# Performance work log

Measured on AMD Instinct MI355X. Metric: run time of the kernel, lower is better.

The kernel has to match this reference:

```python
import jax, jax.numpy as jnp
import numpy as np
import math

B, S, D = 1, 4096, 2048
H, KVH, HD = 16, 4, 128
ROPE_THETA = 10000.0


def _rope_tables(seq_len, head_dim, theta):
    inv_freq = 1.0 / (theta ** (jnp.arange(0, head_dim, 2, dtype=jnp.float32) / head_dim))
    t = jnp.arange(seq_len, dtype=jnp.float32)
    freqs = jnp.outer(t, inv_freq)                      # [S, HD/2]
    emb = jnp.concatenate([freqs, freqs], axis=-1)      # [S, HD]
    return jnp.cos(emb)[None, None], jnp.sin(emb)[None, None]  # [1,1,S,HD]


def setup_inputs() -> dict:
    key = jax.random.key(0)
    ks = jax.random.split(key, 8)
    hidden_states = jax.random.normal(ks[0], (B, S, D), dtype=jnp.float32)
    # additive causal mask [B,1,S,S]
    neg = jnp.finfo(jnp.float32).min
    causal = jnp.where(jnp.tril(jnp.ones((S, S), dtype=bool)), 0.0, neg)
    attention_mask = jnp.broadcast_to(causal[None, None], (B, 1, S, S)).astype(jnp.float32)
    cos, sin = _rope_tables(S, HD, ROPE_THETA)
    gate = jax.random.uniform(ks[1], (B, S), dtype=jnp.float32, minval=0.05, maxval=1.0)
    sc = lambda fan_in: 1.0 / math.sqrt(fan_in)
    Wq = jax.random.normal(ks[2], (D, H * HD), dtype=jnp.float32) * sc(D)
    Wk = jax.random.normal(ks[3], (D, KVH * HD), dtype=jnp.float32) * sc(D)
    Wv = jax.random.normal(ks[4], (D, KVH * HD), dtype=jnp.float32) * sc(D)
    Wo = jax.random.normal(ks[5], (H * HD, D), dtype=jnp.float32) * sc(H * HD)
    return {"hidden_states": hidden_states, "attention_mask": attention_mask,
            "cos": cos, "sin": sin, "gate": gate,
            "Wq": Wq, "Wk": Wk, "Wv": Wv, "Wo": Wo}


def _rotate_half(x):
    h = x.shape[-1] // 2
    return jnp.concatenate([-x[..., h:], x[..., :h]], axis=-1)


def reference(hidden_states, attention_mask, cos, sin, gate, Wq, Wk, Wv, Wo):
    bsz, q_len, _ = hidden_states.shape
    # projections -> [B, heads, S, HD]
    q = (hidden_states @ Wq).reshape(bsz, q_len, H, HD).transpose(0, 2, 1, 3)
    k = (hidden_states @ Wk).reshape(bsz, q_len, KVH, HD).transpose(0, 2, 1, 3)
    v = (hidden_states @ Wv).reshape(bsz, q_len, KVH, HD).transpose(0, 2, 1, 3)
    # inline RoPE
    q = q * cos + _rotate_half(q) * sin
    k = k * cos + _rotate_half(k) * sin
    # GQA: repeat-interleave kv heads to match q heads
    g = H // KVH
    k = jnp.repeat(k, g, axis=1)
    v = jnp.repeat(v, g, axis=1)
    scores = jnp.einsum('bhqd,bhkd->bhqk', q, k) / math.sqrt(HD)
    scores = scores + attention_mask
    scores = scores + jnp.log(gate + 1e-8)[:, None, None, :]  # gate over kv positions
    weights = jax.nn.softmax(scores.astype(jnp.float32), axis=-1).astype(q.dtype)
    out = jnp.einsum('bhqk,bhkd->bhqd', weights, v)
    out = out.transpose(0, 2, 1, 3).reshape(bsz, q_len, H * HD)
    return out @ Wo
```

## Files before the change

### kernel.cpp

```cpp
#include <hip/hip_runtime.h>
#include <math.h>

#define S_LEN 4096
#define DMODEL 2048
#define NH 16
#define NKVH 4
#define HD 128
#define LDQKV 3072

typedef __attribute__((ext_vector_type(4))) float f32x4;
typedef __attribute__((ext_vector_type(8))) short bf16x8;
typedef __attribute__((ext_vector_type(4))) unsigned short us4;

static __device__ __forceinline__ unsigned short f2bf(float f) {
  unsigned int u = __builtin_bit_cast(unsigned int, f);
  u += 0x7fffu + ((u >> 16) & 1u);
  return (unsigned short)(u >> 16);
}
static __device__ __forceinline__ float bf2f(unsigned short h) {
  unsigned int u = ((unsigned int)h) << 16;
  return __builtin_bit_cast(float, u);
}
static __device__ __forceinline__ unsigned int cvt_pk_bf16(float lo, float hi) {
  unsigned int r;
  asm("v_cvt_pk_bf16_f32 %0, %1, %2" : "=v"(r) : "v"(lo), "v"(hi));
  return r;
}

#define GLDS16(g, l) __builtin_amdgcn_global_load_lds( \
    (__attribute__((address_space(1))) void*)(g), \
    (__attribute__((address_space(3))) void*)(l), 16, 0, 0)


__global__ __launch_bounds__(256) void k_cast_bf16(const float* __restrict__ src,
                                                   unsigned short* __restrict__ dst, int n4) {
  int i = blockIdx.x * 256 + threadIdx.x;
  if (i >= n4) return;
  const float4* s = (const float4*)src;
  float4 v = s[i];
  us4 o = { f2bf(v.x), f2bf(v.y), f2bf(v.z), f2bf(v.w) };
  *(us4*)(dst + (size_t)i * 4) = o;
}

__global__ __launch_bounds__(256) void k_transpose_bf16(const float* __restrict__ src,
    unsigned short* __restrict__ dst, int K, int N) {
  __shared__ float tile[64][65];
  int k0 = blockIdx.x * 64, n0 = blockIdx.y * 64;
  int t = threadIdx.x;
#pragma unroll
  for (int i = 0; i < 16; ++i) {
    int idx = t + i * 256;
    int r = idx >> 6, c = idx & 63;
    tile[r][c] = src[(size_t)(k0 + r) * N + n0 + c];
  }
  __syncthreads();
#pragma unroll
  for (int i = 0; i < 16; ++i) {
    int idx = t + i * 256;
    int r = idx >> 6, c = idx & 63;
    dst[(size_t)(n0 + r) * K + k0 + c] = f2bf(tile[c][r]);
  }
}

__global__ __launch_bounds__(256) void k_rope(unsigned short* __restrict__ QKV,
    const float* __restrict__ cp, const float* __restrict__ sp) {
  int gid = blockIdx.x * 256 + threadIdx.x;
  int d = gid & 63;
  int hh = (gid >> 6) % 20;
  int s = gid / 1280;
  int col = hh < NH ? hh * HD : DMODEL + (hh - NH) * HD;
  float qs = hh < NH ? 0.12751589341664477f : 1.0f;
  size_t base = (size_t)s * LDQKV + col;
  float x1 = bf2f(QKV[base + d]);
  float x2 = bf2f(QKV[base + d + 64]);
  float c1 = cp[s * HD + d], s1 = sp[s * HD + d];
  float c2 = cp[s * HD + d + 64], s2 = sp[s * HD + d + 64];
  QKV[base + d]      = f2bf((x1 * c1 - x2 * s1) * qs);
  QKV[base + d + 64] = f2bf((x2 * c2 + x1 * s2) * qs);
}

__global__ __launch_bounds__(256) void k_transpose_v(const unsigned short* __restrict__ QKV,
    unsigned short* __restrict__ Vt) {
  __shared__ unsigned short tile[64][72];
  int s0 = blockIdx.x * 64, c0 = blockIdx.y * 64;
  int t = threadIdx.x;
#pragma unroll
  for (int i = 0; i < 16; ++i) {
    int idx = t + i * 256;
    int r = idx >> 6, c = idx & 63;
    tile[r][c] = QKV[(size_t)(s0 + r) * LDQKV + DMODEL + NKVH * HD + c0 + c];
  }
  __syncthreads();
#pragma unroll
  for (int i = 0; i < 16; ++i) {
    int idx = t + i * 256;
    int r = idx >> 6, c = idx & 63;
    int pc = (c & 3) * 16 + (c >> 2);
    Vt[(size_t)(c0 + r) * S_LEN + s0 + c] = tile[pc][r];
  }
}


template<int OUTF32>
__global__ __launch_bounds__(256) void k_gemm_bt(
    const unsigned short* __restrict__ A, const unsigned short* __restrict__ Bt,
    void* __restrict__ Cp, int M, int N, int K) {
  __shared__ __attribute__((aligned(16))) unsigned short As[128 * 32];
  __shared__ __attribute__((aligned(16))) unsigned short Bs[128 * 32];
  const int t = threadIdx.x;
  const int wave = t >> 6, lane = t & 63;
  const int lr = lane & 15, lg = lane >> 4;
  const int bm = blockIdx.x * 128, bn = blockIdx.y * 128;
  const int wr = (wave >> 1) * 64, wc = (wave & 1) * 64;
  f32x4 acc[4][4];
#pragma unroll
  for (int i = 0; i < 4; ++i)
#pragma unroll
    for (int j = 0; j < 4; ++j) acc[i][j] = (f32x4){0.f, 0.f, 0.f, 0.f};

  for (int k0 = 0; k0 < K; k0 += 32) {
    __syncthreads();
#pragma unroll
    for (int i = 0; i < 2; ++i) {
      const int cb = (wave * 2 + i) * 64;
      const int c = cb + lane;
      const int row = c >> 2, kc = c & 3;
      const int ksw = (kc ^ (row & 3)) * 8;
      GLDS16(A + (size_t)(bm + row) * K + k0 + ksw, (char*)As + cb * 16);
      GLDS16(Bt + (size_t)(bn + row) * K + k0 + ksw, (char*)Bs + cb * 16);
    }
    asm volatile("s_waitcnt vmcnt(0)" ::: "memory");
    __syncthreads();
    bf16x8 af[4], bfr[4];
#pragma unroll
    for (int mi = 0; mi < 4; ++mi) {
      const int row = wr + mi * 16 + lr;
      af[mi] = *(const bf16x8*)(As + row * 32 + ((lg ^ (lr & 3)) * 8));
    }
#pragma unroll
    for (int ni = 0; ni < 4; ++ni) {
      const int row = wc + ni * 16 + lr;
      bfr[ni] = *(const bf16x8*)(Bs + row * 32 + ((lg ^ (lr & 3)) * 8));
    }
#pragma unroll
    for (int mi = 0; mi < 4; ++mi)
#pragma unroll
      for (int ni = 0; ni < 4; ++ni)
        acc[mi][ni] = __builtin_amdgcn_mfma_f32_16x16x32_bf16(af[mi], bfr[ni], acc[mi][ni], 0, 0, 0);
  }
#pragma unroll
  for (int mi = 0; mi < 4; ++mi)
#pragma unroll
    for (int ni = 0; ni < 4; ++ni)
#pragma unroll
      for (int r = 0; r < 4; ++r) {
        const int m = bm + wr + mi * 16 + lg * 4 + r;
        const int n = bn + wc + ni * 16 + lr;
        if (OUTF32) ((float*)Cp)[(size_t)m * N + n] = acc[mi][ni][r];
        else ((unsigned short*)Cp)[(size_t)m * N + n] = f2bf(acc[mi][ni][r]);
      }
}


#define STAGE_KV(kt_, buf_) do { \
  const int kv0_ = (kt_) * 64; \
  _Pragma("unroll") \
  for (int i_ = 0; i_ < 4; ++i_) { \
    const int cb_ = (wave * 4 + i_) * 64; \
    const int c_ = cb_ + lane; \
    { const int row_ = c_ >> 4, kc_ = c_ & 15; \
      GLDS16(Kp + (size_t)(kv0_ + row_) * LDQKV + ((kc_ ^ (row_ & 7)) * 8), \
             (char*)Ks[buf_] + cb_ * 16); } \
    { const int d_ = c_ >> 3, kc_ = c_ & 7; \
      GLDS16(Vp + (size_t)d_ * S_LEN + kv0_ + ((kc_ ^ (d_ & 7)) * 8), \
             (char*)Vs[buf_] + cb_ * 16); } \
  } \
} while (0)

template<bool DIAG>
__device__ __forceinline__ void attn_tile(
    const unsigned short* Kb, const unsigned short* Vb,
    unsigned short (*PsW)[72], const float* __restrict__ gate,
    int kv0, int qbase, const bf16x8* qf,
    f32x4* acc, f32x4& acc_s, float* mrow, int lr, int lg,
    const bf16x8 vb_ones) {
  float g4[4];
#pragma unroll
  for (int cf = 0; cf < 4; ++cf) g4[cf] = gate[kv0 + cf * 16 + lr];

  f32x4 sc[4];
  __builtin_amdgcn_s_setprio(1);
#pragma unroll
  for (int cf = 0; cf < 4; ++cf) {
    sc[cf] = (f32x4){0.f, 0.f, 0.f, 0.f};
    const int row = cf * 16 + lr;
#pragma unroll
    for (int ks = 0; ks < 4; ++ks) {
      bf16x8 kb = *(const bf16x8*)(Kb + row * 128 + (((ks * 4 + lg) ^ (lr & 7)) * 8));
      sc[cf] = __builtin_amdgcn_mfma_f32_16x16x32_bf16(qf[ks], kb, sc[cf], 0, 0, 0);
    }
  }
  __builtin_amdgcn_s_setprio(0);

  if (DIAG) {
#pragma unroll
    for (int cf = 0; cf < 4; ++cf) {
      const int kpos = kv0 + cf * 16 + lr;
#pragma unroll
      for (int r = 0; r < 4; ++r)
        sc[cf][r] = (kpos <= qbase + r) ? sc[cf][r] : -3e38f;
    }
  }
  float lmax[4];
#pragma unroll
  for (int r = 0; r < 4; ++r)
    lmax[r] = fmaxf(fmaxf(sc[0][r], sc[1][r]), fmaxf(sc[2][r], sc[3][r]));

  bool need = (lmax[0] > mrow[0] + 11.5416f) | (lmax[1] > mrow[1] + 11.5416f) |
              (lmax[2] > mrow[2] + 11.5416f) | (lmax[3] > mrow[3] + 11.5416f);
  if (__any(need)) {
    float tm[4] = {lmax[0], lmax[1], lmax[2], lmax[3]};
#pragma unroll
    for (int off = 8; off; off >>= 1)
#pragma unroll
      for (int r = 0; r < 4; ++r) tm[r] = fmaxf(tm[r], __shfl_xor(tm[r], off));
#pragma unroll
    for (int r = 0; r < 4; ++r) {
      const float mn = fmaxf(mrow[r], tm[r]);
      const float alpha = __builtin_amdgcn_exp2f(mrow[r] - mn);
      mrow[r] = mn;
#pragma unroll
      for (int j = 0; j < 8; ++j) acc[j][r] *= alpha;
      acc_s[r] *= alpha;
    }
  }
#pragma unroll
  for (int r = 0; r < 4; ++r) {
    float p0 = __builtin_amdgcn_exp2f(sc[0][r] - mrow[r]) * g4[0];
    float p1 = __builtin_amdgcn_exp2f(sc[1][r] - mrow[r]) * g4[1];
    float p2 = __builtin_amdgcn_exp2f(sc[2][r] - mrow[r]) * g4[2];
    float p3 = __builtin_amdgcn_exp2f(sc[3][r] - mrow[r]) * g4[3];
    uint2 pk = { cvt_pk_bf16(p0, p1), cvt_pk_bf16(p2, p3) };
    *(uint2*)(&PsW[lg * 4 + r][lr * 4]) = pk;
  }
  asm volatile("s_waitcnt lgkmcnt(0)" ::: "memory");
  __builtin_amdgcn_sched_barrier(0);
  __builtin_amdgcn_s_setprio(1);
#pragma unroll
  for (int ks = 0; ks < 2; ++ks) {
    bf16x8 pa = *(const bf16x8*)(&PsW[lr][ks * 32 + lg * 8]);
#pragma unroll
    for (int j = 0; j < 8; ++j) {
      const int d = j * 16 + lr;
      bf16x8 vb = *(const bf16x8*)(Vb + d * 64 + (((ks * 4 + lg) ^ (lr & 7)) * 8));
      acc[j] = __builtin_amdgcn_mfma_f32_16x16x32_bf16(pa, vb, acc[j], 0, 0, 0);
    }
    acc_s = __builtin_amdgcn_mfma_f32_16x16x32_bf16(pa, vb_ones, acc_s, 0, 0, 0);
  }
  __builtin_amdgcn_s_setprio(0);
}

__global__ __launch_bounds__(256) void k_attn(
    const unsigned short* __restrict__ QKV, const unsigned short* __restrict__ Vt,
    const float* __restrict__ gate, unsigned short* __restrict__ Oattn) {
  __shared__ __attribute__((aligned(16))) unsigned short Ks[2][64 * 128];
  __shared__ __attribute__((aligned(16))) unsigned short Vs[2][128 * 64];
  __shared__ __attribute__((aligned(16))) unsigned short Ps[4][16][72];
  const int h = blockIdx.y, kvh = h >> 2;
  const int bx = blockIdx.x;
  const int t = threadIdx.x, wave = t >> 6, lane = t & 63;
  const int lr = lane & 15, lg = lane >> 4;
  const unsigned short* Qp = QKV + h * HD;
  const unsigned short* Kp = QKV + DMODEL + kvh * HD;
  const unsigned short* Vp = Vt + (size_t)kvh * HD * S_LEN;
  unsigned short (*PsW)[72] = Ps[wave];
  bf16x8 vb_ones;
  {
    const short one = (short)0x3F80, z = 0;
    const short e = (lr == 0) ? one : z;
    vb_ones = (bf16x8){e, e, e, e, e, e, e, e};
  }

  for (int half = 0; half < 2; ++half) {
    const int qt = half ? bx : (63 - bx);
    const int q0 = qt * 64;
    const int nt = qt + 1;
    const int qbase = q0 + wave * 16 + lg * 4;

    bf16x8 qf[4];
    {
      const size_t qoff = (size_t)(q0 + wave * 16 + lr) * LDQKV;
#pragma unroll
      for (int ks = 0; ks < 4; ++ks)
        qf[ks] = *(const bf16x8*)(Qp + qoff + ks * 32 + lg * 8);
    }
    f32x4 acc[8];
#pragma unroll
    for (int j = 0; j < 8; ++j) acc[j] = (f32x4){0.f, 0.f, 0.f, 0.f};
    f32x4 acc_s = (f32x4){0.f, 0.f, 0.f, 0.f};
    float mrow[4] = {-3e38f, -3e38f, -3e38f, -3e38f};

    __builtin_amdgcn_s_barrier();
    STAGE_KV(0, 0);

    for (int kt = 0; kt < nt - 1; ++kt) {
      STAGE_KV(kt + 1, (kt + 1) & 1);
      asm volatile("s_waitcnt vmcnt(8)" ::: "memory");
      __builtin_amdgcn_s_barrier();
      attn_tile<false>(Ks[kt & 1], Vs[kt & 1], PsW, gate, kt * 64, qbase,
                       qf, acc, acc_s, mrow, lr, lg, vb_ones);
      __builtin_amdgcn_s_barrier();
    }
    asm volatile("s_waitcnt vmcnt(0)" ::: "memory");
    __builtin_amdgcn_s_barrier();
    attn_tile<true>(Ks[(nt - 1) & 1], Vs[(nt - 1) & 1], PsW, gate, (nt - 1) * 64,
                    qbase, qf, acc, acc_s, mrow, lr, lg, vb_ones);
    __builtin_amdgcn_s_barrier();

    float inv[4];
#pragma unroll
    for (int r = 0; r < 4; ++r)
      inv[r] = 1.0f / __shfl(acc_s[r], lane & 48);
#pragma unroll
    for (int j = 0; j < 8; ++j)
#pragma unroll
      for (int r = 0; r < 4; ++r) {
        const int m = qbase + r;
        Oattn[(size_t)m * DMODEL + h * HD + j * 16 + lr] = f2bf(acc[j][r] * inv[r]);
      }
  }
}


extern "C" void kernel_launch(void* const* d_in, const int* in_sizes, int n_in,
                              void* d_out, int out_size, void* d_ws, size_t ws_size,
                              hipStream_t stream) {
  (void)in_sizes; (void)n_in; (void)out_size; (void)ws_size;
  const float* hid  = (const float*)d_in[0];
  const float* cosp = (const float*)d_in[2];
  const float* sinp = (const float*)d_in[3];
  const float* gate = (const float*)d_in[4];
  const float* Wq   = (const float*)d_in[5];
  const float* Wk   = (const float*)d_in[6];
  const float* Wv   = (const float*)d_in[7];
  const float* Wo   = (const float*)d_in[8];
  float* out = (float*)d_out;
  char* ws = (char*)d_ws;
  unsigned short* Xb   = (unsigned short*)(ws);
  unsigned short* Wt   = (unsigned short*)(ws + (size_t)16777216);
  unsigned short* Wot  = (unsigned short*)(ws + (size_t)29360128);
  unsigned short* QKV  = (unsigned short*)(ws + (size_t)37748736);
  unsigned short* Oatt = (unsigned short*)(ws + (size_t)62914560);
  unsigned short* Vt   = (unsigned short*)(ws + (size_t)79691776);

  k_cast_bf16<<<8192, 256, 0, stream>>>(hid, Xb, 2097152);
  k_transpose_bf16<<<dim3(32, 32), 256, 0, stream>>>(Wq, Wt, 2048, 2048);
  k_transpose_bf16<<<dim3(32, 8), 256, 0, stream>>>(Wk, Wt + (size_t)2048 * 2048, 2048, 512);
  k_transpose_bf16<<<dim3(32, 8), 256, 0, stream>>>(Wv, Wt + (size_t)2560 * 2048, 2048, 512);
  k_transpose_bf16<<<dim3(32, 32), 256, 0, stream>>>(Wo, Wot, 2048, 2048);
  k_gemm_bt<0><<<dim3(32, 24), 256, 0, stream>>>(Xb, Wt, QKV, 4096, 3072, 2048);
  k_rope<<<20480, 256, 0, stream>>>(QKV, cosp, sinp);
  k_transpose_v<<<dim3(64, 8), 256, 0, stream>>>(QKV, Vt);
  k_attn<<<dim3(32, 16), 256, 0, stream>>>(QKV, Vt, gate, Oatt);
  k_gemm_bt<1><<<dim3(32, 16), 256, 0, stream>>>(Oatt, Wot, out, 4096, 2048, 2048);
}
```

Before: 281.0 us.

## Share K/V tiles across paired query tiles in attention and vectorize RoPE

The attention kernel now processes its two query tiles (63-bx and bx) in a single pass over KV. Each staged K/V tile is used for both query tiles until the shorter one finishes, so the early KV tiles are no longer loaded twice per block. The cost is roughly double the register state (two accumulator sets and two Q fragment sets), which may lower occupancy or cause spills. The RoPE kernel is also vectorized to process 4 elements per thread with 8-byte and 16-byte loads, using a quarter as many blocks.

New measurement: 369.5 us. 1.32x slower.

```diff
diff --git a/kernel.cpp b/kernel.cpp
--- a/kernel.cpp
+++ b/kernel.cpp
@@ -65,18 +65,27 @@
 __global__ __launch_bounds__(256) void k_rope(unsigned short* __restrict__ QKV,
     const float* __restrict__ cp, const float* __restrict__ sp) {
   int gid = blockIdx.x * 256 + threadIdx.x;
-  int d = gid & 63;
-  int hh = (gid >> 6) % 20;
-  int s = gid / 1280;
+  int d4 = (gid & 15) * 4;
+  int hh = (gid >> 4) % 20;
+  int s = gid / 320;
   int col = hh < NH ? hh * HD : DMODEL + (hh - NH) * HD;
   float qs = hh < NH ? 0.12751589341664477f : 1.0f;
-  size_t base = (size_t)s * LDQKV + col;
-  float x1 = bf2f(QKV[base + d]);
-  float x2 = bf2f(QKV[base + d + 64]);
-  float c1 = cp[s * HD + d], s1 = sp[s * HD + d];
-  float c2 = cp[s * HD + d + 64], s2 = sp[s * HD + d + 64];
-  QKV[base + d]      = f2bf((x1 * c1 - x2 * s1) * qs);
-  QKV[base + d + 64] = f2bf((x2 * c2 + x1 * s2) * qs);
+  size_t base = (size_t)s * LDQKV + col + d4;
+  us4 x1 = *(us4*)(QKV + base);
+  us4 x2 = *(us4*)(QKV + base + 64);
+  float4 c = *(const float4*)(cp + s * HD + d4);
+  float4 sn = *(const float4*)(sp + s * HD + d4);
+  us4 o1, o2;
+  o1[0] = f2bf((bf2f(x1[0]) * c.x - bf2f(x2[0]) * sn.x) * qs);
+  o1[1] = f2bf((bf2f(x1[1]) * c.y - bf2f(x2[1]) * sn.y) * qs);
+  o1[2] = f2bf((bf2f(x1[2]) * c.z - bf2f(x2[2]) * sn.z) * qs);
+  o1[3] = f2bf((bf2f(x1[3]) * c.w - bf2f(x2[3]) * sn.w) * qs);
+  o2[0] = f2bf((bf2f(x2[0]) * c.x + bf2f(x1[0]) * sn.x) * qs);
+  o2[1] = f2bf((bf2f(x2[1]) * c.y + bf2f(x1[1]) * sn.y) * qs);
+  o2[2] = f2bf((bf2f(x2[2]) * c.z + bf2f(x1[2]) * sn.z) * qs);
+  o2[3] = f2bf((bf2f(x2[3]) * c.w + bf2f(x1[3]) * sn.w) * qs);
+  *(us4*)(QKV + base) = o1;
+  *(us4*)(QKV + base + 64) = o2;
 }
 
 __global__ __launch_bounds__(256) void k_transpose_v(const unsigned short* __restrict__ QKV,
@@ -177,18 +186,26 @@
   } \
 } while (0)
 
-template<bool DIAG>
-__device__ __forceinline__ void attn_tile(
-    const unsigned short* Kb, const unsigned short* Vb,
-    unsigned short (*PsW)[72], const float* __restrict__ gate,
-    int kv0, int qbase, const bf16x8* qf,
-    f32x4* acc, f32x4& acc_s, float* mrow, int lr, int lg,
-    const bf16x8 vb_ones) {
-  float g4[4];
-#pragma unroll
-  for (int cf = 0; cf < 4; ++cf) g4[cf] = gate[kv0 + cf * 16 + lr];
-
-  f32x4 sc[4];
+__device__ __forceinline__ void qkt_pair(const unsigned short* Kb,
+    const bf16x8* qfA, const bf16x8* qfB, f32x4* scA, f32x4* scB, int lr, int lg) {
+  __builtin_amdgcn_s_setprio(1);
+#pragma unroll
+  for (int cf = 0; cf < 4; ++cf) {
+    scA[cf] = (f32x4){0.f, 0.f, 0.f, 0.f};
+    scB[cf] = (f32x4){0.f, 0.f, 0.f, 0.f};
+    const int row = cf * 16 + lr;
+#pragma unroll
+    for (int ks = 0; ks < 4; ++ks) {
+      bf16x8 kb = *(const bf16x8*)(Kb + row * 128 + (((ks * 4 + lg) ^ (lr & 7)) * 8));
+      scA[cf] = __builtin_amdgcn_mfma_f32_16x16x32_bf16(qfA[ks], kb, scA[cf], 0, 0, 0);
+      scB[cf] = __builtin_amdgcn_mfma_f32_16x16x32_bf16(qfB[ks], kb, scB[cf], 0, 0, 0);
+    }
+  }
+  __builtin_amdgcn_s_setprio(0);
+}
+
+__device__ __forceinline__ void qkt_one(const unsigned short* Kb,
+    const bf16x8* qf, f32x4* sc, int lr, int lg) {
   __builtin_amdgcn_s_setprio(1);
 #pragma unroll
   for (int cf = 0; cf < 4; ++cf) {
@@ -201,7 +218,14 @@
     }
   }
   __builtin_amdgcn_s_setprio(0);
-
+}
+
+template<bool DIAG>
+__device__ __forceinline__ void softmax_pv(
+    f32x4* sc, const unsigned short* Vb, unsigned short (*PsW)[72],
+    const float* g4, int kv0, int qbase,
+    f32x4* acc, f32x4& acc_s, float* mrow, int lr, int lg,
+    const bf16x8 vb_ones) {
   if (DIAG) {
 #pragma unroll
     for (int cf = 0; cf < 4; ++cf) {
@@ -281,54 +305,99 @@
     vb_ones = (bf16x8){e, e, e, e, e, e, e, e};
   }
 
-  for (int half = 0; half < 2; ++half) {
-    const int qt = half ? bx : (63 - bx);
-    const int q0 = qt * 64;
-    const int nt = qt + 1;
-    const int qbase = q0 + wave * 16 + lg * 4;
-
-    bf16x8 qf[4];
-    {
-      const size_t qoff = (size_t)(q0 + wave * 16 + lr) * LDQKV;
-#pragma unroll
-      for (int ks = 0; ks < 4; ++ks)
-        qf[ks] = *(const bf16x8*)(Qp + qoff + ks * 32 + lg * 8);
-    }
-    f32x4 acc[8];
-#pragma unroll
-    for (int j = 0; j < 8; ++j) acc[j] = (f32x4){0.f, 0.f, 0.f, 0.f};
-    f32x4 acc_s = (f32x4){0.f, 0.f, 0.f, 0.f};
-    float mrow[4] = {-3e38f, -3e38f, -3e38f, -3e38f};
-
-    __builtin_amdgcn_s_barrier();
-    STAGE_KV(0, 0);
-
-    for (int kt = 0; kt < nt - 1; ++kt) {
-      STAGE_KV(kt + 1, (kt + 1) & 1);
-      asm volatile("s_waitcnt vmcnt(8)" ::: "memory");
-      __builtin_amdgcn_s_barrier();
-      attn_tile<false>(Ks[kt & 1], Vs[kt & 1], PsW, gate, kt * 64, qbase,
-                       qf, acc, acc_s, mrow, lr, lg, vb_ones);
-      __builtin_amdgcn_s_barrier();
-    }
+  const int qtA = 63 - bx, qtB = bx;
+  const int qbaseA = qtA * 64 + wave * 16 + lg * 4;
+  const int qbaseB = qtB * 64 + wave * 16 + lg * 4;
+
+  bf16x8 qfA[4], qfB[4];
+  {
+    const size_t offA = (size_t)(qtA * 64 + wave * 16 + lr) * LDQKV;
+    const size_t offB = (size_t)(qtB * 64 + wave * 16 + lr) * LDQKV;
+#pragma unroll
+    for (int ks = 0; ks < 4; ++ks) {
+      qfA[ks] = *(const bf16x8*)(Qp + offA + ks * 32 + lg * 8);
+      qfB[ks] = *(const bf16x8*)(Qp + offB + ks * 32 + lg * 8);
+    }
+  }
+  f32x4 accA[8], accB[8];
+#pragma unroll
+  for (int j = 0; j < 8; ++j) {
+    accA[j] = (f32x4){0.f, 0.f, 0.f, 0.f};
+    accB[j] = (f32x4){0.f, 0.f, 0.f, 0.f};
+  }
+  f32x4 acc_sA = (f32x4){0.f, 0.f, 0.f, 0.f};
+  f32x4 acc_sB = (f32x4){0.f, 0.f, 0.f, 0.f};
+  float mrowA[4] = {-3e38f, -3e38f, -3e38f, -3e38f};
+  float mrowB[4] = {-3e38f, -3e38f, -3e38f, -3e38f};
+
+  STAGE_KV(0, 0);
+
+  f32x4 scA[4], scB[4];
+  float g4[4];
+  int kt = 0;
+  for (; kt < qtB; ++kt) {
+    STAGE_KV(kt + 1, (kt + 1) & 1);
+    asm volatile("s_waitcnt vmcnt(8)" ::: "memory");
+    __builtin_amdgcn_s_barrier();
+    const unsigned short* Kb = Ks[kt & 1];
+    const unsigned short* Vb = Vs[kt & 1];
+#pragma unroll
+    for (int cf = 0; cf < 4; ++cf) g4[cf] = gate[kt * 64 + cf * 16 + lr];
+    qkt_pair(Kb, qfA, qfB, scA, scB, lr, lg);
+    softmax_pv<false>(scA, Vb, PsW, g4, kt * 64, qbaseA, accA, acc_sA, mrowA, lr, lg, vb_ones);
+    softmax_pv<false>(scB, Vb, PsW, g4, kt * 64, qbaseB, accB, acc_sB, mrowB, lr, lg, vb_ones);
+    __builtin_amdgcn_s_barrier();
+  }
+  {
+    STAGE_KV(kt + 1, (kt + 1) & 1);
+    asm volatile("s_waitcnt vmcnt(8)" ::: "memory");
+    __builtin_amdgcn_s_barrier();
+    const unsigned short* Kb = Ks[kt & 1];
+    const unsigned short* Vb = Vs[kt & 1];
+#pragma unroll
+    for (int cf = 0; cf < 4; ++cf) g4[cf] = gate[kt * 64 + cf * 16 + lr];
+    qkt_pair(Kb, qfA, qfB, scA, scB, lr, lg);
+    softmax_pv<false>(scA, Vb, PsW, g4, kt * 64, qbaseA, accA, acc_sA, mrowA, lr, lg, vb_ones);
+    softmax_pv<true>(scB, Vb, PsW, g4, kt * 64, qbaseB, accB, acc_sB, mrowB, lr, lg, vb_ones);
+    __builtin_amdgcn_s_barrier();
+    ++kt;
+  }
+  for (; kt < qtA; ++kt) {
+    STAGE_KV(kt + 1, (kt + 1) & 1);
+    asm volatile("s_waitcnt vmcnt(8)" ::: "memory");
+    __builtin_amdgcn_s_barrier();
+    const unsigned short* Kb = Ks[kt & 1];
+    const unsigned short* Vb = Vs[kt & 1];
+#pragma unroll
+    for (int cf = 0; cf < 4; ++cf) g4[cf] = gate[kt * 64 + cf * 16 + lr];
+    qkt_one(Kb, qfA, scA, lr, lg);
+    softmax_pv<false>(scA, Vb, PsW, g4, kt * 64, qbaseA, accA, acc_sA, mrowA, lr, lg, vb_ones);
+    __builtin_amdgcn_s_barrier();
+  }
+  {
     asm volatile("s_waitcnt vmcnt(0)" ::: "memory");
     __builtin_amdgcn_s_barrier();
-    attn_tile<true>(Ks[(nt - 1) & 1], Vs[(nt - 1) & 1], PsW, gate, (nt - 1) * 64,
-                    qbase, qf, acc, acc_s, mrow, lr, lg, vb_ones);
-    __builtin_amdgcn_s_barrier();
-
-    float inv[4];
-#pragma unroll
-    for (int r = 0; r < 4; ++r)
-      inv[r] = 1.0f / __shfl(acc_s[r], lane & 48);
-#pragma unroll
-    for (int j = 0; j < 8; ++j)
-#pragma unroll
-      for (int r = 0; r < 4; ++r) {
-        const int m = qbase + r;
-        Oattn[(size_t)m * DMODEL + h * HD + j * 16 + lr] = f2bf(acc[j][r] * inv[r]);
-      }
-  }
+    const unsigned short* Kb = Ks[kt & 1];
+    const unsigned short* Vb = Vs[kt & 1];
+#pragma unroll
+    for (int cf = 0; cf < 4; ++cf) g4[cf] = gate[kt * 64 + cf * 16 + lr];
+    qkt_one(Kb, qfA, scA, lr, lg);
+    softmax_pv<true>(scA, Vb, PsW, g4, kt * 64, qbaseA, accA, acc_sA, mrowA, lr, lg, vb_ones);
+  }
+
+  float invA[4], invB[4];
+#pragma unroll
+  for (int r = 0; r < 4; ++r) {
+    invA[r] = 1.0f / __shfl(acc_sA[r], lane & 48);
+    invB[r] = 1.0f / __shfl(acc_sB[r], lane & 48);
+  }
+#pragma unroll
+  for (int j = 0; j < 8; ++j)
+#pragma unroll
+    for (int r = 0; r < 4; ++r) {
+      Oattn[(size_t)(qbaseA + r) * DMODEL + h * HD + j * 16 + lr] = f2bf(accA[j][r] * invA[r]);
+      Oattn[(size_t)(qbaseB + r) * DMODEL + h * HD + j * 16 + lr] = f2bf(accB[j][r] * invB[r]);
+    }
 }
 
 
@@ -359,7 +428,7 @@
   k_transpose_bf16<<<dim3(32, 8), 256, 0, stream>>>(Wv, Wt + (size_t)2560 * 2048, 2048, 512);
   k_transpose_bf16<<<dim3(32, 32), 256, 0, stream>>>(Wo, Wot, 2048, 2048);
   k_gemm_bt<0><<<dim3(32, 24), 256, 0, stream>>>(Xb, Wt, QKV, 4096, 3072, 2048);
-  k_rope<<<20480, 256, 0, stream>>>(QKV, cosp, sinp);
+  k_rope<<<5120, 256, 0, stream>>>(QKV, cosp, sinp);
   k_transpose_v<<<dim3(64, 8), 256, 0, stream>>>(QKV, Vt);
   k_attn<<<dim3(32, 16), 256, 0, stream>>>(QKV, Vt, gate, Oatt);
   k_gemm_bt<1><<<dim3(32, 16), 256, 0, stream>>>(Oatt, Wot, out, 4096, 2048, 2048);
```

## Double attention query tile to 128 rows with 8 waves; vectorize RoPE

Applied to the files above, without the earlier changes.

The attention kernel now processes 128 query rows per block using 512 threads (8 waves), so each staged K/V tile is shared by twice as many query rows. This halves the number of blocks and the global K/V traffic per query. The last two KV tiles are handled specially for the causal diagonal, and waves whose rows end before the final tile skip it. RoPE is vectorized to process 4 elements per thread with 64-bit and 128-bit loads. Risks are lower occupancy and fewer blocks to balance across CUs, plus more barrier cost with 8 waves.

New measurement: 284.3 us. No clear change (+1.2%).

```diff
diff --git a/kernel.cpp b/kernel.cpp
--- a/kernel.cpp
+++ b/kernel.cpp
@@ -65,18 +65,27 @@
 __global__ __launch_bounds__(256) void k_rope(unsigned short* __restrict__ QKV,
     const float* __restrict__ cp, const float* __restrict__ sp) {
   int gid = blockIdx.x * 256 + threadIdx.x;
-  int d = gid & 63;
-  int hh = (gid >> 6) % 20;
-  int s = gid / 1280;
+  int d4 = (gid & 15) * 4;
+  int hh = (gid >> 4) % 20;
+  int s = gid / 320;
   int col = hh < NH ? hh * HD : DMODEL + (hh - NH) * HD;
   float qs = hh < NH ? 0.12751589341664477f : 1.0f;
-  size_t base = (size_t)s * LDQKV + col;
-  float x1 = bf2f(QKV[base + d]);
-  float x2 = bf2f(QKV[base + d + 64]);
-  float c1 = cp[s * HD + d], s1 = sp[s * HD + d];
-  float c2 = cp[s * HD + d + 64], s2 = sp[s * HD + d + 64];
-  QKV[base + d]      = f2bf((x1 * c1 - x2 * s1) * qs);
-  QKV[base + d + 64] = f2bf((x2 * c2 + x1 * s2) * qs);
+  size_t base = (size_t)s * LDQKV + col + d4;
+  us4 x1 = *(us4*)(QKV + base);
+  us4 x2 = *(us4*)(QKV + base + 64);
+  float4 c = *(const float4*)(cp + s * HD + d4);
+  float4 sn = *(const float4*)(sp + s * HD + d4);
+  us4 o1, o2;
+  o1[0] = f2bf((bf2f(x1[0]) * c.x - bf2f(x2[0]) * sn.x) * qs);
+  o1[1] = f2bf((bf2f(x1[1]) * c.y - bf2f(x2[1]) * sn.y) * qs);
+  o1[2] = f2bf((bf2f(x1[2]) * c.z - bf2f(x2[2]) * sn.z) * qs);
+  o1[3] = f2bf((bf2f(x1[3]) * c.w - bf2f(x2[3]) * sn.w) * qs);
+  o2[0] = f2bf((bf2f(x2[0]) * c.x + bf2f(x1[0]) * sn.x) * qs);
+  o2[1] = f2bf((bf2f(x2[1]) * c.y + bf2f(x1[1]) * sn.y) * qs);
+  o2[2] = f2bf((bf2f(x2[2]) * c.z + bf2f(x1[2]) * sn.z) * qs);
+  o2[3] = f2bf((bf2f(x2[3]) * c.w + bf2f(x1[3]) * sn.w) * qs);
+  *(us4*)(QKV + base) = o1;
+  *(us4*)(QKV + base + 64) = o2;
 }
 
 __global__ __launch_bounds__(256) void k_transpose_v(const unsigned short* __restrict__ QKV,
@@ -165,8 +174,8 @@
 #define STAGE_KV(kt_, buf_) do { \
   const int kv0_ = (kt_) * 64; \
   _Pragma("unroll") \
-  for (int i_ = 0; i_ < 4; ++i_) { \
-    const int cb_ = (wave * 4 + i_) * 64; \
+  for (int i_ = 0; i_ < 2; ++i_) { \
+    const int cb_ = (wave * 2 + i_) * 64; \
     const int c_ = cb_ + lane; \
     { const int row_ = c_ >> 4, kc_ = c_ & 15; \
       GLDS16(Kp + (size_t)(kv0_ + row_) * LDQKV + ((kc_ ^ (row_ & 7)) * 8), \
@@ -177,18 +186,8 @@
   } \
 } while (0)
 
-template<bool DIAG>
-__device__ __forceinline__ void attn_tile(
-    const unsigned short* Kb, const unsigned short* Vb,
-    unsigned short (*PsW)[72], const float* __restrict__ gate,
-    int kv0, int qbase, const bf16x8* qf,
-    f32x4* acc, f32x4& acc_s, float* mrow, int lr, int lg,
-    const bf16x8 vb_ones) {
-  float g4[4];
-#pragma unroll
-  for (int cf = 0; cf < 4; ++cf) g4[cf] = gate[kv0 + cf * 16 + lr];
-
-  f32x4 sc[4];
+__device__ __forceinline__ void qkt_one(const unsigned short* Kb,
+    const bf16x8* qf, f32x4* sc, int lr, int lg) {
   __builtin_amdgcn_s_setprio(1);
 #pragma unroll
   for (int cf = 0; cf < 4; ++cf) {
@@ -201,7 +200,14 @@
     }
   }
   __builtin_amdgcn_s_setprio(0);
-
+}
+
+template<bool DIAG>
+__device__ __forceinline__ void softmax_pv(
+    f32x4* sc, const unsigned short* Vb, unsigned short (*PsW)[72],
+    const float* g4, int kv0, int qbase,
+    f32x4* acc, f32x4& acc_s, float* mrow, int lr, int lg,
+    const bf16x8 vb_ones) {
   if (DIAG) {
 #pragma unroll
     for (int cf = 0; cf < 4; ++cf) {
@@ -260,12 +266,12 @@
   __builtin_amdgcn_s_setprio(0);
 }
 
-__global__ __launch_bounds__(256) void k_attn(
+__global__ __launch_bounds__(512) void k_attn(
     const unsigned short* __restrict__ QKV, const unsigned short* __restrict__ Vt,
     const float* __restrict__ gate, unsigned short* __restrict__ Oattn) {
   __shared__ __attribute__((aligned(16))) unsigned short Ks[2][64 * 128];
   __shared__ __attribute__((aligned(16))) unsigned short Vs[2][128 * 64];
-  __shared__ __attribute__((aligned(16))) unsigned short Ps[4][16][72];
+  __shared__ __attribute__((aligned(16))) unsigned short Ps[8][16][72];
   const int h = blockIdx.y, kvh = h >> 2;
   const int bx = blockIdx.x;
   const int t = threadIdx.x, wave = t >> 6, lane = t & 63;
@@ -282,10 +288,11 @@
   }
 
   for (int half = 0; half < 2; ++half) {
-    const int qt = half ? bx : (63 - bx);
-    const int q0 = qt * 64;
-    const int nt = qt + 1;
+    const int st = half ? bx : (31 - bx);
+    const int q0 = st * 128;
+    const int nt = st * 2 + 2;
     const int qbase = q0 + wave * 16 + lg * 4;
+    const int wrow_last = q0 + wave * 16 + 15;
 
     bf16x8 qf[4];
     {
@@ -299,23 +306,45 @@
     for (int j = 0; j < 8; ++j) acc[j] = (f32x4){0.f, 0.f, 0.f, 0.f};
     f32x4 acc_s = (f32x4){0.f, 0.f, 0.f, 0.f};
     float mrow[4] = {-3e38f, -3e38f, -3e38f, -3e38f};
+    f32x4 sc[4];
+    float g4[4];
 
     __builtin_amdgcn_s_barrier();
     STAGE_KV(0, 0);
 
-    for (int kt = 0; kt < nt - 1; ++kt) {
+    int kt = 0;
+    for (; kt < nt - 2; ++kt) {
       STAGE_KV(kt + 1, (kt + 1) & 1);
-      asm volatile("s_waitcnt vmcnt(8)" ::: "memory");
-      __builtin_amdgcn_s_barrier();
-      attn_tile<false>(Ks[kt & 1], Vs[kt & 1], PsW, gate, kt * 64, qbase,
-                       qf, acc, acc_s, mrow, lr, lg, vb_ones);
-      __builtin_amdgcn_s_barrier();
-    }
-    asm volatile("s_waitcnt vmcnt(0)" ::: "memory");
-    __builtin_amdgcn_s_barrier();
-    attn_tile<true>(Ks[(nt - 1) & 1], Vs[(nt - 1) & 1], PsW, gate, (nt - 1) * 64,
-                    qbase, qf, acc, acc_s, mrow, lr, lg, vb_ones);
-    __builtin_amdgcn_s_barrier();
+      asm volatile("s_waitcnt vmcnt(4)" ::: "memory");
+      __builtin_amdgcn_s_barrier();
+#pragma unroll
+      for (int cf = 0; cf < 4; ++cf) g4[cf] = gate[kt * 64 + cf * 16 + lr];
+      qkt_one(Ks[kt & 1], qf, sc, lr, lg);
+      softmax_pv<false>(sc, Vs[kt & 1], PsW, g4, kt * 64, qbase, acc, acc_s, mrow, lr, lg, vb_ones);
+      __builtin_amdgcn_s_barrier();
+    }
+    {
+      STAGE_KV(kt + 1, (kt + 1) & 1);
+      asm volatile("s_waitcnt vmcnt(4)" ::: "memory");
+      __builtin_amdgcn_s_barrier();
+#pragma unroll
+      for (int cf = 0; cf < 4; ++cf) g4[cf] = gate[kt * 64 + cf * 16 + lr];
+      qkt_one(Ks[kt & 1], qf, sc, lr, lg);
+      softmax_pv<true>(sc, Vs[kt & 1], PsW, g4, kt * 64, qbase, acc, acc_s, mrow, lr, lg, vb_ones);
+      __builtin_amdgcn_s_barrier();
+      ++kt;
+    }
+    {
+      const int kv0 = kt * 64;
+      asm volatile("s_waitcnt vmcnt(0)" ::: "memory");
+      __builtin_amdgcn_s_barrier();
+      if (kv0 <= wrow_last) {
+#pragma unroll
+        for (int cf = 0; cf < 4; ++cf) g4[cf] = gate[kv0 + cf * 16 + lr];
+        qkt_one(Ks[kt & 1], qf, sc, lr, lg);
+        softmax_pv<true>(sc, Vs[kt & 1], PsW, g4, kv0, qbase, acc, acc_s, mrow, lr, lg, vb_ones);
+      }
+    }
 
     float inv[4];
 #pragma unroll
@@ -324,10 +353,8 @@
 #pragma unroll
     for (int j = 0; j < 8; ++j)
 #pragma unroll
-      for (int r = 0; r < 4; ++r) {
-        const int m = qbase + r;
-        Oattn[(size_t)m * DMODEL + h * HD + j * 16 + lr] = f2bf(acc[j][r] * inv[r]);
-      }
+      for (int r = 0; r < 4; ++r)
+        Oattn[(size_t)(qbase + r) * DMODEL + h * HD + j * 16 + lr] = f2bf(acc[j][r] * inv[r]);
   }
 }
 
@@ -359,8 +386,8 @@
   k_transpose_bf16<<<dim3(32, 8), 256, 0, stream>>>(Wv, Wt + (size_t)2560 * 2048, 2048, 512);
   k_transpose_bf16<<<dim3(32, 32), 256, 0, stream>>>(Wo, Wot, 2048, 2048);
   k_gemm_bt<0><<<dim3(32, 24), 256, 0, stream>>>(Xb, Wt, QKV, 4096, 3072, 2048);
-  k_rope<<<20480, 256, 0, stream>>>(QKV, cosp, sinp);
+  k_rope<<<5120, 256, 0, stream>>>(QKV, cosp, sinp);
   k_transpose_v<<<dim3(64, 8), 256, 0, stream>>>(QKV, Vt);
-  k_attn<<<dim3(32, 16), 256, 0, stream>>>(QKV, Vt, gate, Oatt);
+  k_attn<<<dim3(16, 16), 512, 0, stream>>>(QKV, Vt, gate, Oatt);
   k_gemm_bt<1><<<dim3(32, 16), 256, 0, stream>>>(Oatt, Wot, out, 4096, 2048, 2048);
 }
```
